# Kernel tuning notes

Measured on AMD Instinct MI355X. Metric: run time of the kernel, lower is better.

The kernel has to match this reference:

```python
import jax, jax.numpy as jnp
import numpy as np

B, T, E, H = 64, 320, 1024, 16
HS = E // H  # 64
EPS = 1e-5


def layernorm(x, w, b):
    mu = jnp.mean(x, axis=-1, keepdims=True)
    var = jnp.mean((x - mu) ** 2, axis=-1, keepdims=True)
    return (x - mu) * jax.lax.rsqrt(var + EPS) * w + b


def setup_inputs() -> dict:
    key = jax.random.key(0)
    ks = jax.random.split(key, 12)
    s_e = 1.0 / np.sqrt(E)
    s_f = 1.0 / np.sqrt(4 * E)
    return {
        "x": jax.random.normal(ks[0], (B, T, E), jnp.float32),
        "Wq": jax.random.uniform(ks[1], (H, E, HS), jnp.float32, -s_e, s_e),
        "Wk": jax.random.uniform(ks[2], (H, E, HS), jnp.float32, -s_e, s_e),
        "Wv": jax.random.uniform(ks[3], (H, E, HS), jnp.float32, -s_e, s_e),
        "Wo": jax.random.uniform(ks[4], (E, E), jnp.float32, -s_e, s_e),
        "bo": jax.random.uniform(ks[5], (E,), jnp.float32, -s_e, s_e),
        "W1": jax.random.uniform(ks[6], (E, 4 * E), jnp.float32, -s_e, s_e),
        "b1": jax.random.uniform(ks[7], (4 * E,), jnp.float32, -s_e, s_e),
        "W2": jax.random.uniform(ks[8], (4 * E, E), jnp.float32, -s_f, s_f),
        "b2": jax.random.uniform(ks[9], (E,), jnp.float32, -s_f, s_f),
        "ln1_w": jnp.ones((E,), jnp.float32),
        "ln1_b": jnp.zeros((E,), jnp.float32),
        "ln2_w": jnp.ones((E,), jnp.float32),
        "ln2_b": jnp.zeros((E,), jnp.float32),
    }


def reference(x, Wq, Wk, Wv, Wo, bo, W1, b1, W2, b2, ln1_w, ln1_b, ln2_w, ln2_b):
    # --- self-attention sublayer (dropout = identity in eval) ---
    h = layernorm(x, ln1_w, ln1_b)
    q = jnp.einsum("bte,hed->bhtd", h, Wq)
    k = jnp.einsum("bte,hed->bhtd", h, Wk)
    v = jnp.einsum("bte,hed->bhtd", h, Wv)
    # NOTE: original scales by full embedding dim C=E, not head_size
    scores = jnp.einsum("bhtd,bhsd->bhts", q, k) * (E ** -0.5)
    causal = jnp.tril(jnp.ones((T, T), bool))
    scores = jnp.where(causal, scores, -jnp.inf)
    wei = jax.nn.softmax(scores, axis=-1)
    attn = jnp.einsum("bhts,bhsd->bthd", wei, v).reshape(B, T, E)
    x = x + attn @ Wo + bo
    # --- feed-forward sublayer ---
    h2 = layernorm(x, ln2_w, ln2_b)
    x = x + jax.nn.relu(h2 @ W1 + b1) @ W2 + b2
    return x
```

## Files before the change

### kernel.cpp

```cpp
#include <hip/hip_runtime.h>


#define B_ 64
#define T_ 320
#define E_ 1024
#define H_ 16
#define HS_ 64
#define NTOK (B_ * T_)

typedef __attribute__((ext_vector_type(8))) __bf16 bf16x8;
typedef __attribute__((ext_vector_type(4))) float f32x4;

__device__ __forceinline__ unsigned short f2bf(float f) {
    unsigned u = __builtin_bit_cast(unsigned, f);
    u += 0x7fffu + ((u >> 16) & 1u);
    return (unsigned short)(u >> 16);
}
__device__ __forceinline__ float bf2f(unsigned short b) {
    return __builtin_bit_cast(float, (unsigned)b << 16);
}

__global__ __launch_bounds__(256) void ln_kernel(const float* __restrict__ x,
                                                 const float* __restrict__ w,
                                                 const float* __restrict__ b,
                                                 unsigned short* __restrict__ y) {
    int row = blockIdx.x;
    int t = threadIdx.x;
    const float4* xr = (const float4*)(x + (size_t)row * E_);
    float4 v = xr[t];
    float s = v.x + v.y + v.z + v.w;
    float s2 = v.x * v.x + v.y * v.y + v.z * v.z + v.w * v.w;
#pragma unroll
    for (int o = 1; o < 64; o <<= 1) {
        s += __shfl_xor(s, o);
        s2 += __shfl_xor(s2, o);
    }
    __shared__ float rs[4], rs2[4];
    int wv = t >> 6;
    if ((t & 63) == 0) { rs[wv] = s; rs2[wv] = s2; }
    __syncthreads();
    s = rs[0] + rs[1] + rs[2] + rs[3];
    s2 = rs2[0] + rs2[1] + rs2[2] + rs2[3];
    float mu = s * (1.0f / E_);
    float var = s2 * (1.0f / E_) - mu * mu;
    float inv = rsqrtf(var + 1e-5f);
    float4 w4 = ((const float4*)w)[t];
    float4 b4 = ((const float4*)b)[t];
    ushort4 o4;
    o4.x = f2bf((v.x - mu) * inv * w4.x + b4.x);
    o4.y = f2bf((v.y - mu) * inv * w4.y + b4.y);
    o4.z = f2bf((v.z - mu) * inv * w4.z + b4.z);
    o4.w = f2bf((v.w - mu) * inv * w4.w + b4.w);
    *(ushort4*)(y + (size_t)row * E_ + 4 * t) = o4;
}

__global__ __launch_bounds__(256) void tcast_kernel(const float* __restrict__ src,
                                                    unsigned short* __restrict__ dst,
                                                    int K, int N, long sStride, long dStride) {
    src += (size_t)blockIdx.z * sStride;
    dst += (size_t)blockIdx.z * dStride;
    __shared__ float tile[64][65];
    int k0 = blockIdx.y * 64, n0 = blockIdx.x * 64;
    int tx = threadIdx.x & 63, ty = threadIdx.x >> 6;
#pragma unroll
    for (int r = ty; r < 64; r += 4)
        tile[r][tx] = src[(size_t)(k0 + r) * N + n0 + tx];
    __syncthreads();
#pragma unroll
    for (int r = ty; r < 64; r += 4)
        dst[(size_t)(n0 + r) * K + k0 + tx] = f2bf(tile[tx][r]);
}

template <bool BF16OUT, bool BIAS, bool RELU, bool RESID>
__global__ __launch_bounds__(256)
void gemm_mfma(const unsigned short* __restrict__ A,
               const unsigned short* __restrict__ Bt,
               const float* __restrict__ bias,
               const float* __restrict__ resid,
               void* __restrict__ Cout, int K, int N) {
    __shared__ uint4 A4[128 * 4];
    __shared__ uint4 B4[128 * 4];
    const int tid = threadIdx.x;
    const int lane = tid & 63;
    const int wave = tid >> 6;
    const int wr = wave >> 1, wc = wave & 1;
    const int m0 = blockIdx.y * 128;
    const int n0 = blockIdx.x * 128;
    const int r16 = lane & 15;
    const int s = lane >> 4;
    const int sw = s ^ ((r16 >> 1) & 3);

    const int ar0 = tid >> 2, as0 = tid & 3;
    const int asw = as0 ^ ((ar0 >> 1) & 3);
    const unsigned short* Ag = A + (size_t)(m0 + ar0) * K + as0 * 8;
    const unsigned short* Bg = Bt + (size_t)(n0 + ar0) * K + as0 * 8;
    const size_t rowSkip = (size_t)64 * K;

    f32x4 acc[4][4];
#pragma unroll
    for (int i = 0; i < 4; i++)
#pragma unroll
        for (int j = 0; j < 4; j++) acc[i][j] = (f32x4){0.f, 0.f, 0.f, 0.f};

    const bf16x8* Ab = (const bf16x8*)A4;
    const bf16x8* Bb = (const bf16x8*)B4;

    for (int k0 = 0; k0 < K; k0 += 32) {
        uint4 a0 = *(const uint4*)(Ag + k0);
        uint4 a1 = *(const uint4*)(Ag + rowSkip + k0);
        uint4 b0 = *(const uint4*)(Bg + k0);
        uint4 b1 = *(const uint4*)(Bg + rowSkip + k0);
        __syncthreads();
        A4[(ar0 << 2) + asw] = a0;
        A4[((ar0 + 64) << 2) + asw] = a1;
        B4[(ar0 << 2) + asw] = b0;
        B4[((ar0 + 64) << 2) + asw] = b1;
        __syncthreads();
        bf16x8 af[4], bf[4];
#pragma unroll
        for (int i = 0; i < 4; i++) {
            af[i] = Ab[(((wr << 6) + (i << 4) + r16) << 2) + sw];
            bf[i] = Bb[(((wc << 6) + (i << 4) + r16) << 2) + sw];
        }
#pragma unroll
        for (int i = 0; i < 4; i++)
#pragma unroll
            for (int j = 0; j < 4; j++)
                acc[i][j] = __builtin_amdgcn_mfma_f32_16x16x32_bf16(af[i], bf[j], acc[i][j], 0, 0, 0);
    }

    const int crow0 = m0 + wr * 64;
    const int ccol0 = n0 + wc * 64;
#pragma unroll
    for (int j = 0; j < 4; j++) {
        int gcol = ccol0 + j * 16 + r16;
        float bv = BIAS ? bias[gcol] : 0.f;
#pragma unroll
        for (int i = 0; i < 4; i++) {
            int growb = crow0 + i * 16 + s * 4;
#pragma unroll
            for (int r = 0; r < 4; r++) {
                float vo = acc[i][j][r] + bv;
                if (RELU) vo = fmaxf(vo, 0.f);
                int grow = growb + r;
                if (RESID) vo += resid[(size_t)grow * N + gcol];
                if (BF16OUT)
                    ((unsigned short*)Cout)[(size_t)grow * N + gcol] = f2bf(vo);
                else
                    ((float*)Cout)[(size_t)grow * N + gcol] = vo;
            }
        }
    }
}

__global__ __launch_bounds__(256) void attn_mfma(const unsigned short* __restrict__ qkv,
                                                 unsigned short* __restrict__ attn) {
    const int it = blockIdx.x;
    const int bh = blockIdx.y;
    const int b = bh >> 4, head = bh & 15;
    __shared__ uint4 KsV[512];
    __shared__ uint4 VtV[512];
    __shared__ uint4 PsV[4][128];
    unsigned short* Ks = (unsigned short*)KsV;
    unsigned short* Vt = (unsigned short*)VtV;

    const int tid = threadIdx.x;
    const int lane = tid & 63;
    const int w = tid >> 6;
    const int r16 = lane & 15;
    const int s = lane >> 4;
    unsigned short* P = (unsigned short*)PsV[w];

    const int qg = it * 64 + w * 16 + r16;
    const size_t qrow = (size_t)(b * T_ + qg) * 3072;

    bf16x8 qf0 = *(const bf16x8*)(qkv + qrow + head * 64 + 0 * 32 + s * 8);
    bf16x8 qf1 = *(const bf16x8*)(qkv + qrow + head * 64 + 1 * 32 + s * 8);

    f32x4 accO[4];
#pragma unroll
    for (int i = 0; i < 4; i++) accO[i] = (f32x4){0.f, 0.f, 0.f, 0.f};
    float m = -1e30f, l = 0.f;

    for (int j = 0; j <= it; j++) {
        __syncthreads();
#pragma unroll
        for (int half = 0; half < 2; half++) {
            int cid = tid + half * 256;
            int row = cid >> 3, sl = cid & 7;
            size_t tok = (size_t)(b * T_ + j * 64 + row) * 3072 + head * 64 + sl * 8;
            uint4 kc = *(const uint4*)(qkv + tok + 1024);
            uint4 vc = *(const uint4*)(qkv + tok + 2048);
            *(uint4*)(Ks + row * 64 + ((sl ^ (row & 7)) * 8)) = kc;
            union { uint4 u; unsigned short h[8]; } vv; vv.u = vc;
#pragma unroll
            for (int e = 0; e < 8; e++) {
                int d = sl * 8 + e;
                Vt[d * 64 + (((row >> 3) ^ (d & 7)) * 8) + (row & 7)] = vv.h[e];
            }
        }
        __syncthreads();

        f32x4 accS[4];
#pragma unroll
        for (int i = 0; i < 4; i++) accS[i] = (f32x4){0.f, 0.f, 0.f, 0.f};
#pragma unroll
        for (int c = 0; c < 2; c++) {
            bf16x8 qc = c ? qf1 : qf0;
#pragma unroll
            for (int i = 0; i < 4; i++) {
                int kvr = i * 16 + r16;
                bf16x8 kf = *(const bf16x8*)(Ks + kvr * 64 + (((c * 4 + s) ^ (kvr & 7)) * 8));
                accS[i] = __builtin_amdgcn_mfma_f32_16x16x32_bf16(kf, qc, accS[i], 0, 0, 0);
            }
        }

        float sv[16];
        float smax = -1e30f;
#pragma unroll
        for (int i = 0; i < 4; i++)
#pragma unroll
            for (int r = 0; r < 4; r++) {
                float vsc = accS[i][r] * 0.03125f;
                int kvg = j * 64 + i * 16 + 4 * s + r;
                if (kvg > qg) vsc = -1e30f;
                sv[i * 4 + r] = vsc;
                smax = fmaxf(smax, vsc);
            }
        smax = fmaxf(smax, __shfl_xor(smax, 16));
        smax = fmaxf(smax, __shfl_xor(smax, 32));
        float mn = fmaxf(m, smax);
        float al = __expf(m - mn);
        float ps = 0.f;
        unsigned short pb[16];
#pragma unroll
        for (int idx = 0; idx < 16; idx++) {
            float p = __expf(sv[idx] - mn);
            ps += p;
            pb[idx] = f2bf(p);
        }
        ps += __shfl_xor(ps, 16);
        ps += __shfl_xor(ps, 32);
        l = l * al + ps;
        m = mn;
#pragma unroll
        for (int i = 0; i < 4; i++)
#pragma unroll
            for (int r = 0; r < 4; r++) accO[i][r] *= al;

#pragma unroll
        for (int i = 0; i < 4; i++)
#pragma unroll
            for (int r = 0; r < 4; r++) {
                int kv = i * 16 + 4 * s + r;
                P[r16 * 64 + (((kv >> 3) ^ (r16 & 7)) * 8) + (kv & 7)] = pb[i * 4 + r];
            }
        asm volatile("s_waitcnt lgkmcnt(0)" ::: "memory");

#pragma unroll
        for (int c = 0; c < 2; c++) {
            bf16x8 pf = *(const bf16x8*)(P + r16 * 64 + (((c * 4 + s) ^ (r16 & 7)) * 8));
#pragma unroll
            for (int i = 0; i < 4; i++) {
                int d = i * 16 + r16;
                bf16x8 vf = *(const bf16x8*)(Vt + d * 64 + (((c * 4 + s) ^ (d & 7)) * 8));
                accO[i] = __builtin_amdgcn_mfma_f32_16x16x32_bf16(vf, pf, accO[i], 0, 0, 0);
            }
        }
    }

    float inv = 1.0f / l;
#pragma unroll
    for (int i = 0; i < 4; i++)
#pragma unroll
        for (int r = 0; r < 4; r++) {
            int d = i * 16 + 4 * s + r;
            P[r16 * 64 + (((d >> 3) ^ (r16 & 7)) * 8) + (d & 7)] = f2bf(accO[i][r] * inv);
        }
    asm volatile("s_waitcnt lgkmcnt(0)" ::: "memory");
#pragma unroll
    for (int half = 0; half < 2; half++) {
        int cid = lane + half * 64;
        int row = cid >> 3, sl = cid & 7;
        uint4 o = *(const uint4*)(P + row * 64 + ((sl ^ (row & 7)) * 8));
        *(uint4*)(attn + (size_t)(b * T_ + it * 64 + w * 16 + row) * E_ + head * 64 + sl * 8) = o;
    }
}

extern "C" void kernel_launch(void* const* d_in, const int* in_sizes, int n_in,
                              void* d_out, int out_size, void* d_ws, size_t ws_size,
                              hipStream_t stream) {
    const float* x    = (const float*)d_in[0];
    const float* Wq   = (const float*)d_in[1];
    const float* Wk   = (const float*)d_in[2];
    const float* Wv   = (const float*)d_in[3];
    const float* Wo   = (const float*)d_in[4];
    const float* bo   = (const float*)d_in[5];
    const float* W1   = (const float*)d_in[6];
    const float* b1   = (const float*)d_in[7];
    const float* W2   = (const float*)d_in[8];
    const float* b2   = (const float*)d_in[9];
    const float* ln1w = (const float*)d_in[10];
    const float* ln1b = (const float*)d_in[11];
    const float* ln2w = (const float*)d_in[12];
    const float* ln2b = (const float*)d_in[13];
    float* out = (float*)d_out;

    unsigned short* ws = (unsigned short*)d_ws;
    unsigned short* qkvWt = ws;
    unsigned short* WoT   = qkvWt + 3072 * 1024;
    unsigned short* W1T   = WoT + 1024 * 1024;
    unsigned short* W2T   = W1T + 4096 * 1024;
    unsigned short* hbuf  = W2T + 1024 * 4096;
    unsigned short* qkv   = hbuf + (size_t)NTOK * E_;
    unsigned short* abuf  = qkv + (size_t)NTOK * 3 * E_;
    unsigned short* inter = qkv;

    tcast_kernel<<<dim3(1, 16, 16), 256, 0, stream>>>(Wq, qkvWt, E_, HS_,
                                                      (long)E_ * HS_, (long)HS_ * E_);
    tcast_kernel<<<dim3(1, 16, 16), 256, 0, stream>>>(Wk, qkvWt + 1024 * 1024, E_, HS_,
                                                      (long)E_ * HS_, (long)HS_ * E_);
    tcast_kernel<<<dim3(1, 16, 16), 256, 0, stream>>>(Wv, qkvWt + 2048 * 1024, E_, HS_,
                                                      (long)E_ * HS_, (long)HS_ * E_);
    tcast_kernel<<<dim3(16, 16, 1), 256, 0, stream>>>(Wo, WoT, E_, E_, 0, 0);
    tcast_kernel<<<dim3(64, 16, 1), 256, 0, stream>>>(W1, W1T, E_, 4 * E_, 0, 0);
    tcast_kernel<<<dim3(16, 64, 1), 256, 0, stream>>>(W2, W2T, 4 * E_, E_, 0, 0);

    ln_kernel<<<NTOK, 256, 0, stream>>>(x, ln1w, ln1b, hbuf);
    gemm_mfma<true, false, false, false><<<dim3(24, 160), 256, 0, stream>>>(
        hbuf, qkvWt, nullptr, nullptr, qkv, 1024, 3072);
    attn_mfma<<<dim3(T_ / 64, B_ * H_), 256, 0, stream>>>(qkv, abuf);
    gemm_mfma<false, true, false, true><<<dim3(8, 160), 256, 0, stream>>>(
        abuf, WoT, bo, x, out, 1024, 1024);
    ln_kernel<<<NTOK, 256, 0, stream>>>(out, ln2w, ln2b, hbuf);
    gemm_mfma<true, true, true, false><<<dim3(32, 160), 256, 0, stream>>>(
        hbuf, W1T, b1, nullptr, inter, 1024, 4096);
    gemm_mfma<false, true, false, true><<<dim3(8, 160), 256, 0, stream>>>(
        inter, W2T, b2, out, out, 4096, 1024);
}
```

Baseline: 1.139 ms.

## Load GEMM tiles directly into LDS and swizzle block order

The GEMM tile staging now uses global_load_lds, so each wave copies 16-byte chunks straight from global memory into shared memory instead of going through VGPRs. The XOR swizzle moves from the LDS write address to the global read address. Workgroup IDs are also remapped into eight interleaved groups to change L2 reuse across neighbouring blocks. This frees registers and instructions for staging, but the loop is still single-buffered and correctness depends on the barrier waiting for the LDS DMA to complete.

```diff
diff --git a/kernel.cpp b/kernel.cpp
--- a/kernel.cpp
+++ b/kernel.cpp
@@ -18,6 +18,11 @@
 }
 __device__ __forceinline__ float bf2f(unsigned short b) {
     return __builtin_bit_cast(float, (unsigned)b << 16);
+}
+__device__ __forceinline__ void gload16(const void* g, void* l) {
+    __builtin_amdgcn_global_load_lds(
+        (const __attribute__((address_space(1))) unsigned int*)g,
+        (__attribute__((address_space(3))) unsigned int*)l, 16, 0, 0);
 }
 
 __global__ __launch_bounds__(256) void ln_kernel(const float* __restrict__ x,
@@ -80,21 +85,33 @@
                void* __restrict__ Cout, int K, int N) {
     __shared__ uint4 A4[128 * 4];
     __shared__ uint4 B4[128 * 4];
+    const int total = gridDim.x * gridDim.y;
+    const int flat = blockIdx.y * gridDim.x + blockIdx.x;
+    const int cpx = total >> 3;
+    const int swz = (flat & 7) * cpx + (flat >> 3);
+    const int m0 = (swz / gridDim.x) * 128;
+    const int n0 = (swz % gridDim.x) * 128;
+
     const int tid = threadIdx.x;
     const int lane = tid & 63;
     const int wave = tid >> 6;
     const int wr = wave >> 1, wc = wave & 1;
-    const int m0 = blockIdx.y * 128;
-    const int n0 = blockIdx.x * 128;
     const int r16 = lane & 15;
     const int s = lane >> 4;
     const int sw = s ^ ((r16 >> 1) & 3);
 
-    const int ar0 = tid >> 2, as0 = tid & 3;
-    const int asw = as0 ^ ((ar0 >> 1) & 3);
-    const unsigned short* Ag = A + (size_t)(m0 + ar0) * K + as0 * 8;
-    const unsigned short* Bg = Bt + (size_t)(n0 + ar0) * K + as0 * 8;
-    const size_t rowSkip = (size_t)64 * K;
+    const int rin = lane >> 2;
+    const int sl = lane & 3;
+    const int gsl = sl ^ ((rin >> 1) & 3);
+    const int rowA = wave * 32 + rin;
+    const unsigned short* Ag0 = A + (size_t)(m0 + rowA) * K + gsl * 8;
+    const unsigned short* Ag1 = Ag0 + (size_t)16 * K;
+    const unsigned short* Bg0 = Bt + (size_t)(n0 + rowA) * K + gsl * 8;
+    const unsigned short* Bg1 = Bg0 + (size_t)16 * K;
+    uint4* ldsA0 = &A4[(wave * 32) * 4];
+    uint4* ldsA1 = &A4[(wave * 32 + 16) * 4];
+    uint4* ldsB0 = &B4[(wave * 32) * 4];
+    uint4* ldsB1 = &B4[(wave * 32 + 16) * 4];
 
     f32x4 acc[4][4];
 #pragma unroll
@@ -106,15 +123,11 @@
     const bf16x8* Bb = (const bf16x8*)B4;
 
     for (int k0 = 0; k0 < K; k0 += 32) {
-        uint4 a0 = *(const uint4*)(Ag + k0);
-        uint4 a1 = *(const uint4*)(Ag + rowSkip + k0);
-        uint4 b0 = *(const uint4*)(Bg + k0);
-        uint4 b1 = *(const uint4*)(Bg + rowSkip + k0);
         __syncthreads();
-        A4[(ar0 << 2) + asw] = a0;
-        A4[((ar0 + 64) << 2) + asw] = a1;
-        B4[(ar0 << 2) + asw] = b0;
-        B4[((ar0 + 64) << 2) + asw] = b1;
+        gload16(Ag0 + k0, ldsA0);
+        gload16(Ag1 + k0, ldsA1);
+        gload16(Bg0 + k0, ldsB0);
+        gload16(Bg1 + k0, ldsB1);
         __syncthreads();
         bf16x8 af[4], bf[4];
 #pragma unroll
```

After: 1.141 ms. Within noise of the previous version (+0.2%).
